# Kernel tuning notes

Measured on AMD Instinct MI355X. Metric: run time of the kernel, lower is better.

Reference implementation:

```python
import jax, jax.numpy as jnp
import numpy as np

IN_F = 8192
OUT_F = 8192
TOKENS = 4096
QP = 127.0   # 2**(8-1) - 1
QN = -128.0  # -2**(8-1)


def setup_inputs() -> dict:
    key = jax.random.key(0)
    k1, k2 = jax.random.split(key)
    x = jax.random.normal(k1, (TOKENS, IN_F), dtype=jnp.float32)
    # torch.randint(0, 2, ...) -> values in {0, 1}
    weight = jax.random.randint(k2, (OUT_F, IN_F), 0, 2, dtype=jnp.int32)
    weight_scale = jnp.ones((1,), dtype=jnp.float32)
    bias = jnp.zeros((OUT_F,), dtype=jnp.float32)
    return {"x": x, "weight": weight, "weight_scale": weight_scale, "bias": bias}


def reference(x, weight, weight_scale, bias):
    # activation_quant: per-row symmetric int8 quantization
    s = QP / jnp.clip(jnp.max(jnp.abs(x), axis=-1, keepdims=True), 1e-5)  # [T,1]
    x_q = jnp.clip(jnp.round(x * s), QN, QP)  # int8 values held in f32 (exact)
    y = jnp.einsum('tk,nk->tn', x_q, weight.astype(x.dtype))  # [T, OUT_F]
    # post_quant_process: dequantize by activation scale then weight scale
    out = y / s / weight_scale
    return out + bias[None, :]
```

## Files before the change

kernel.cpp:

```cpp
#include <hip/hip_runtime.h>

#define TOKENS 4096
#define IN_F   8192
#define OUT_F  8192
#define BK     64
#define TILEB  24576
#define NT     (IN_F / BK)

typedef int v4i __attribute__((ext_vector_type(4)));

__device__ __forceinline__ void gload_lds16(const void* g, void* l) {
    __builtin_amdgcn_global_load_lds(
        (const __attribute__((address_space(1))) void*)g,
        (__attribute__((address_space(3))) void*)l, 16, 0, 0);
}

__global__ __launch_bounds__(256) void quant_kernel(const float* __restrict__ x,
                                                    signed char* __restrict__ xq,
                                                    float* __restrict__ recip_s) {
    const int row = blockIdx.x;
    const int t   = threadIdx.x;
    const float4* xr = (const float4*)(x + (size_t)row * IN_F);
    float4 v[8];
    float m = 0.f;
#pragma unroll
    for (int i = 0; i < 8; ++i) {
        v[i] = xr[t + 256 * i];
        m = fmaxf(m, fmaxf(fmaxf(fabsf(v[i].x), fabsf(v[i].y)),
                           fmaxf(fabsf(v[i].z), fabsf(v[i].w))));
    }
#pragma unroll
    for (int off = 32; off > 0; off >>= 1)
        m = fmaxf(m, __shfl_xor(m, off));
    __shared__ float wmax[4];
    if ((t & 63) == 0) wmax[t >> 6] = m;
    __syncthreads();
    m = fmaxf(fmaxf(wmax[0], wmax[1]), fmaxf(wmax[2], wmax[3]));
    m = fmaxf(m, 1e-5f);
    const float s = 127.0f / m;
    if (t == 0) recip_s[row] = m / 127.0f;
    unsigned int* out = (unsigned int*)(xq + (size_t)row * IN_F);
#pragma unroll
    for (int i = 0; i < 8; ++i) {
        int a = (int)fminf(fmaxf(rintf(v[i].x * s), -128.f), 127.f);
        int b = (int)fminf(fmaxf(rintf(v[i].y * s), -128.f), 127.f);
        int c = (int)fminf(fmaxf(rintf(v[i].z * s), -128.f), 127.f);
        int d = (int)fminf(fmaxf(rintf(v[i].w * s), -128.f), 127.f);
        out[t + 256 * i] = (a & 255) | ((b & 255) << 8) | ((c & 255) << 16) | ((d & 255) << 24);
    }
}

__global__ __launch_bounds__(256) void pack_w(const int* __restrict__ w,
                                              unsigned int* __restrict__ w8) {
    const size_t idx = (size_t)blockIdx.x * 256 + threadIdx.x;
    int4 a = ((const int4*)w)[idx];
    w8[idx] = (a.x & 255) | ((a.y & 255) << 8) | ((a.z & 255) << 16) | ((a.w & 255) << 24);
}

__global__ __launch_bounds__(256, 2) void gemm_kernel(const signed char* __restrict__ A,
                                                      const signed char* __restrict__ B,
                                                      const float* __restrict__ recip_s,
                                                      const float* __restrict__ wscale,
                                                      const float* __restrict__ bias,
                                                      float* __restrict__ out) {
    __shared__ signed char smem[3 * TILEB];
    const int t    = threadIdx.x;
    const int wave = t >> 6;
    const int lane = t & 63;
    const int m0 = blockIdx.y * 128;
    const int n0 = blockIdx.x * 256;
    const int wm = (wave >> 1) * 64;
    const int wn = (wave & 1) * 128;

    v4i acc[4][8] = {};

    const int rowS = t >> 2;
    const int colS = ((t & 3) ^ ((t >> 3) & 3)) * 16;
    const signed char* gA = A + (size_t)(m0 + rowS) * IN_F + colS;
    const signed char* gB = B + (size_t)(n0 + rowS) * IN_F + colS;

    const int r16 = lane & 15;
    const int q   = lane >> 4;
    const int cOff = ((q ^ ((r16 >> 1) & 3)) * 16);

#define STAGE(kt, buf) do {                                                  \
        signed char* lA = smem + (buf) * TILEB + t * 16;                     \
        signed char* lB = lA + 8192;                                         \
        const size_t k0 = (size_t)(kt) * BK;                                 \
        gload_lds16(gA + k0, lA);                                            \
        gload_lds16(gA + (size_t)64  * IN_F + k0, lA + 4096);                \
        gload_lds16(gB + k0, lB);                                            \
        gload_lds16(gB + (size_t)64  * IN_F + k0, lB + 4096);                \
        gload_lds16(gB + (size_t)128 * IN_F + k0, lB + 8192);                \
        gload_lds16(gB + (size_t)192 * IN_F + k0, lB + 12288);               \
    } while (0)

#define COMPUTE(buf) do {                                                    \
        const signed char* As_ = smem + (buf) * TILEB;                       \
        const signed char* Bs_ = As_ + 8192;                                 \
        v4i a[4], b[8];                                                      \
        _Pragma("unroll")                                                    \
        for (int i = 0; i < 4; ++i)                                          \
            a[i] = *(const v4i*)(As_ + (wm + i * 16 + r16) * 64 + cOff);     \
        _Pragma("unroll")                                                    \
        for (int j = 0; j < 8; ++j)                                          \
            b[j] = *(const v4i*)(Bs_ + (wn + j * 16 + r16) * 64 + cOff);     \
        __builtin_amdgcn_s_setprio(1);                                       \
        _Pragma("unroll")                                                    \
        for (int i = 0; i < 4; ++i)                                          \
            _Pragma("unroll")                                                \
            for (int j = 0; j < 8; ++j)                                      \
                acc[i][j] = __builtin_amdgcn_mfma_i32_16x16x64_i8(           \
                    a[i], b[j], acc[i][j], 0, 0, 0);                         \
        __builtin_amdgcn_s_setprio(0);                                       \
    } while (0)

#define WAITBAR(N) do {                                                      \
        asm volatile("s_waitcnt vmcnt(" #N ")" ::: "memory");                \
        __builtin_amdgcn_s_barrier();                                        \
        asm volatile("" ::: "memory");                                       \
    } while (0)

    STAGE(0, 0);
    asm volatile("s_waitcnt vmcnt(0)" ::: "memory");
    STAGE(1, 1);
    __builtin_amdgcn_s_barrier();
    asm volatile("" ::: "memory");

    for (int kt = 0; kt < NT - 2; kt += 3) {
        STAGE(kt + 2, 2); COMPUTE(0); WAITBAR(6);
        STAGE(kt + 3, 0); COMPUTE(1); WAITBAR(6);
        STAGE(kt + 4, 1); COMPUTE(2); WAITBAR(6);
    }
    COMPUTE(0);
    WAITBAR(0);
    COMPUTE(1);

#undef STAGE
#undef COMPUTE
#undef WAITBAR

    const float rws = 1.0f / wscale[0];
#pragma unroll
    for (int i = 0; i < 4; ++i) {
#pragma unroll
        for (int r = 0; r < 4; ++r) {
            const int row = m0 + wm + i * 16 + q * 4 + r;
            const float rs = recip_s[row] * rws;
#pragma unroll
            for (int j = 0; j < 8; ++j) {
                const int col = n0 + wn + j * 16 + r16;
                out[(size_t)row * OUT_F + col] = (float)acc[i][j][r] * rs + bias[col];
            }
        }
    }
}

extern "C" void kernel_launch(void* const* d_in, const int* in_sizes, int n_in,
                              void* d_out, int out_size, void* d_ws, size_t ws_size,
                              hipStream_t stream) {
    const float* x      = (const float*)d_in[0];
    const int*   w      = (const int*)d_in[1];
    const float* wscale = (const float*)d_in[2];
    const float* bias   = (const float*)d_in[3];
    float* out = (float*)d_out;

    signed char* xq = (signed char*)d_ws;
    signed char* w8 = xq + (size_t)TOKENS * IN_F;
    float* recip_s  = (float*)(w8 + (size_t)OUT_F * IN_F);

    quant_kernel<<<TOKENS, 256, 0, stream>>>(x, xq, recip_s);
    pack_w<<<(int)(((size_t)OUT_F * IN_F) / 4 / 256), 256, 0, stream>>>(w, (unsigned int*)w8);
    dim3 grid(OUT_F / 256, TOKENS / 128);
    gemm_kernel<<<grid, 256, 0, stream>>>(xq, w8, recip_s, wscale, bias, out);
}
```

Baseline: 699.1 us.

## Enlarge GEMM tile to 256x256 with 32x32 MFMA and register double-buffering

Each block now computes a 256x256 output tile, up from 128x256, so each loaded A/B byte is reused more. The 16x16x64 int8 MFMA is replaced by 32x32x32 with 128x128 per-wave subtiles. LDS fragment loads are software-pipelined into alternating register sets so the next tile's reads overlap the current MFMAs. The launch is flattened to a 1D grid with an XCD/L2-aware swizzle, and bias is hoisted into registers. In exchange occupancy drops to one block per CU, with more registers and 96KB of LDS per block.

```diff
diff --git a/kernel.cpp b/kernel.cpp
--- a/kernel.cpp
+++ b/kernel.cpp
@@ -4,10 +4,11 @@
 #define IN_F   8192
 #define OUT_F  8192
 #define BK     64
-#define TILEB  24576
+#define TILEB  32768
 #define NT     (IN_F / BK)
 
-typedef int v4i __attribute__((ext_vector_type(4)));
+typedef int v4i  __attribute__((ext_vector_type(4)));
+typedef int v16i __attribute__((ext_vector_type(16)));
 
 __device__ __forceinline__ void gload_lds16(const void* g, void* l) {
     __builtin_amdgcn_global_load_lds(
@@ -57,7 +58,7 @@
     w8[idx] = (a.x & 255) | ((a.y & 255) << 8) | ((a.z & 255) << 16) | ((a.w & 255) << 24);
 }
 
-__global__ __launch_bounds__(256, 2) void gemm_kernel(const signed char* __restrict__ A,
+__global__ __launch_bounds__(256, 1) void gemm_kernel(const signed char* __restrict__ A,
                                                       const signed char* __restrict__ B,
                                                       const float* __restrict__ recip_s,
                                                       const float* __restrict__ wscale,
@@ -67,90 +68,119 @@
     const int t    = threadIdx.x;
     const int wave = t >> 6;
     const int lane = t & 63;
-    const int m0 = blockIdx.y * 128;
-    const int n0 = blockIdx.x * 256;
-    const int wm = (wave >> 1) * 64;
+
+    const int bid = blockIdx.x;
+    const int swz = (bid & 7) * 64 + (bid >> 3);
+    const int m0  = (swz & 15) * 256;
+    const int n0  = (swz >> 4) * 256;
+
+    const int wm = (wave >> 1) * 128;
     const int wn = (wave & 1) * 128;
 
-    v4i acc[4][8] = {};
+    v16i acc[4][4] = {};
 
     const int rowS = t >> 2;
     const int colS = ((t & 3) ^ ((t >> 3) & 3)) * 16;
     const signed char* gA = A + (size_t)(m0 + rowS) * IN_F + colS;
     const signed char* gB = B + (size_t)(n0 + rowS) * IN_F + colS;
 
-    const int r16 = lane & 15;
-    const int q   = lane >> 4;
-    const int cOff = ((q ^ ((r16 >> 1) & 3)) * 16);
-
-#define STAGE(kt, buf) do {                                                  \
-        signed char* lA = smem + (buf) * TILEB + t * 16;                     \
-        signed char* lB = lA + 8192;                                         \
-        const size_t k0 = (size_t)(kt) * BK;                                 \
-        gload_lds16(gA + k0, lA);                                            \
-        gload_lds16(gA + (size_t)64  * IN_F + k0, lA + 4096);                \
-        gload_lds16(gB + k0, lB);                                            \
-        gload_lds16(gB + (size_t)64  * IN_F + k0, lB + 4096);                \
-        gload_lds16(gB + (size_t)128 * IN_F + k0, lB + 8192);                \
-        gload_lds16(gB + (size_t)192 * IN_F + k0, lB + 12288);               \
-    } while (0)
-
-#define COMPUTE(buf) do {                                                    \
-        const signed char* As_ = smem + (buf) * TILEB;                       \
-        const signed char* Bs_ = As_ + 8192;                                 \
-        v4i a[4], b[8];                                                      \
+    const int l31 = lane & 31;
+    const int q5  = lane >> 5;
+    const int s   = (l31 >> 1) & 3;
+    const int aO0 = (wm + l31) * 64 + (((0 + q5) ^ s) * 16);
+    const int aO1 = (wm + l31) * 64 + (((2 + q5) ^ s) * 16);
+    const int bO0 = 16384 + (wn + l31) * 64 + (((0 + q5) ^ s) * 16);
+    const int bO1 = 16384 + (wn + l31) * 64 + (((2 + q5) ^ s) * 16);
+
+    v4i aF0[8], bF0[8], aF1[8], bF1[8];
+
+#define STAGE(kt, b3) do {                                                   \
+        signed char* l0 = smem + (b3) * TILEB + t * 16;                      \
+        const size_t ko = (size_t)(kt) * BK;                                 \
+        gload_lds16(gA + ko,                        l0);                     \
+        gload_lds16(gA + (size_t)64  * IN_F + ko,   l0 + 4096);              \
+        gload_lds16(gA + (size_t)128 * IN_F + ko,   l0 + 8192);              \
+        gload_lds16(gA + (size_t)192 * IN_F + ko,   l0 + 12288);             \
+        gload_lds16(gB + ko,                        l0 + 16384);             \
+        gload_lds16(gB + (size_t)64  * IN_F + ko,   l0 + 20480);             \
+        gload_lds16(gB + (size_t)128 * IN_F + ko,   l0 + 24576);             \
+        gload_lds16(gB + (size_t)192 * IN_F + ko,   l0 + 28672);             \
+    } while (0)
+
+#define FRAGS(b3, aF, bF) do {                                               \
+        const signed char* bp = smem + (b3) * TILEB;                         \
         _Pragma("unroll")                                                    \
-        for (int i = 0; i < 4; ++i)                                          \
-            a[i] = *(const v4i*)(As_ + (wm + i * 16 + r16) * 64 + cOff);     \
-        _Pragma("unroll")                                                    \
-        for (int j = 0; j < 8; ++j)                                          \
-            b[j] = *(const v4i*)(Bs_ + (wn + j * 16 + r16) * 64 + cOff);     \
+        for (int i = 0; i < 4; ++i) {                                        \
+            aF[i * 2 + 0] = *(const v4i*)(bp + aO0 + i * 2048);              \
+            aF[i * 2 + 1] = *(const v4i*)(bp + aO1 + i * 2048);              \
+            bF[i * 2 + 0] = *(const v4i*)(bp + bO0 + i * 2048);              \
+            bF[i * 2 + 1] = *(const v4i*)(bp + bO1 + i * 2048);              \
+        }                                                                    \
+    } while (0)
+
+#define MM(aF, bF) do {                                                      \
         __builtin_amdgcn_s_setprio(1);                                       \
         _Pragma("unroll")                                                    \
-        for (int i = 0; i < 4; ++i)                                          \
+        for (int kk = 0; kk < 2; ++kk)                                       \
             _Pragma("unroll")                                                \
-            for (int j = 0; j < 8; ++j)                                      \
-                acc[i][j] = __builtin_amdgcn_mfma_i32_16x16x64_i8(           \
-                    a[i], b[j], acc[i][j], 0, 0, 0);                         \
+            for (int i = 0; i < 4; ++i)                                      \
+                _Pragma("unroll")                                            \
+                for (int j = 0; j < 4; ++j)                                  \
+                    acc[i][j] = __builtin_amdgcn_mfma_i32_32x32x32_i8(       \
+                        aF[i * 2 + kk], bF[j * 2 + kk], acc[i][j], 0, 0, 0); \
         __builtin_amdgcn_s_setprio(0);                                       \
     } while (0)
 
-#define WAITBAR(N) do {                                                      \
-        asm volatile("s_waitcnt vmcnt(" #N ")" ::: "memory");                \
+#define BODY(kt, b3s, b3f, aN, bN, aC, bC) do {                              \
+        STAGE((kt) + 2, b3s);                                                \
+        asm volatile("s_waitcnt vmcnt(8)" ::: "memory");                     \
         __builtin_amdgcn_s_barrier();                                        \
         asm volatile("" ::: "memory");                                       \
+        FRAGS(b3f, aN, bN);                                                  \
+        MM(aC, bC);                                                          \
     } while (0)
 
     STAGE(0, 0);
-    asm volatile("s_waitcnt vmcnt(0)" ::: "memory");
     STAGE(1, 1);
+    asm volatile("s_waitcnt vmcnt(8)" ::: "memory");
     __builtin_amdgcn_s_barrier();
     asm volatile("" ::: "memory");
-
-    for (int kt = 0; kt < NT - 2; kt += 3) {
-        STAGE(kt + 2, 2); COMPUTE(0); WAITBAR(6);
-        STAGE(kt + 3, 0); COMPUTE(1); WAITBAR(6);
-        STAGE(kt + 4, 1); COMPUTE(2); WAITBAR(6);
-    }
-    COMPUTE(0);
-    WAITBAR(0);
-    COMPUTE(1);
+    FRAGS(0, aF0, bF0);
+
+    for (int kt = 0; kt < NT - 2; kt += 6) {
+        BODY(kt + 0, 2, 1, aF1, bF1, aF0, bF0);
+        BODY(kt + 1, 0, 2, aF0, bF0, aF1, bF1);
+        BODY(kt + 2, 1, 0, aF1, bF1, aF0, bF0);
+        BODY(kt + 3, 2, 1, aF0, bF0, aF1, bF1);
+        BODY(kt + 4, 0, 2, aF1, bF1, aF0, bF0);
+        BODY(kt + 5, 1, 0, aF0, bF0, aF1, bF1);
+    }
+    asm volatile("s_waitcnt vmcnt(0)" ::: "memory");
+    __builtin_amdgcn_s_barrier();
+    asm volatile("" ::: "memory");
+    FRAGS(1, aF1, bF1);
+    MM(aF0, bF0);
+    MM(aF1, bF1);
 
 #undef STAGE
-#undef COMPUTE
-#undef WAITBAR
+#undef FRAGS
+#undef MM
+#undef BODY
 
     const float rws = 1.0f / wscale[0];
+    float bj[4];
+#pragma unroll
+    for (int j = 0; j < 4; ++j) bj[j] = bias[n0 + wn + j * 32 + l31];
 #pragma unroll
     for (int i = 0; i < 4; ++i) {
 #pragma unroll
-        for (int r = 0; r < 4; ++r) {
-            const int row = m0 + wm + i * 16 + q * 4 + r;
+        for (int r = 0; r < 16; ++r) {
+            const int row = m0 + wm + i * 32 + (r & 3) + 8 * (r >> 2) + 4 * q5;
             const float rs = recip_s[row] * rws;
 #pragma unroll
-            for (int j = 0; j < 8; ++j) {
-                const int col = n0 + wn + j * 16 + r16;
-                out[(size_t)row * OUT_F + col] = (float)acc[i][j][r] * rs + bias[col];
+            for (int j = 0; j < 4; ++j) {
+                const int col = n0 + wn + j * 32 + l31;
+                out[(size_t)row * OUT_F + col] = (float)acc[i][j][r] * rs + bj[j];
             }
         }
     }
@@ -171,6 +201,5 @@
 
     quant_kernel<<<TOKENS, 256, 0, stream>>>(x, xq, recip_s);
     pack_w<<<(int)(((size_t)OUT_F * IN_F) / 4 / 256), 256, 0, stream>>>(w, (unsigned int*)w8);
-    dim3 grid(OUT_F / 256, TOKENS / 128);
-    gemm_kernel<<<grid, 256, 0, stream>>>(xq, w8, recip_s, wscale, bias, out);
-}
+    gemm_kernel<<<(TOKENS / 256) * (OUT_F / 256), 256, 0, stream>>>(xq, w8, recip_s, wscale, bias, out);
+}
```

Result: slower. 740.3 us (+5.9%).
